# Kernel optimization log

Hardware: AMD Instinct MI355X
Metric: run time of the kernel (lower is better)

The kernel has to match this reference:

```python
import jax, jax.numpy as jnp
import numpy as np

BATCH, L = 2, 1024
D_MODEL, D_INNER, D_STATE, DT_RANK, K = 2048, 4096, 16, 128, 4


def setup_inputs() -> dict:
    key = jax.random.key(0)
    ks = jax.random.split(key, 9)
    g = lambda i, shape, s: jax.random.normal(ks[i], shape, jnp.float32) * s
    A_log = jnp.log(jnp.broadcast_to(jnp.arange(1, D_STATE + 1, dtype=jnp.float32),
                                     (D_INNER, D_STATE)))
    return {
        "hidden_states": g(0, (BATCH, L, D_MODEL), 1.0),
        "W_in": g(1, (2 * D_INNER, D_MODEL), 0.02),
        "conv_w": g(2, (D_INNER, K), 0.2),
        "conv_b": g(3, (D_INNER,), 0.02),
        "W_x": g(4, (DT_RANK + 2 * D_STATE, D_INNER), 0.02),
        "W_dt": g(5, (D_INNER, DT_RANK), 0.02),
        "b_dt": g(6, (D_INNER,), 0.02),
        "A_log": A_log,
        "D": jnp.ones((D_INNER,), jnp.float32),
        "W_out": g(7, (D_MODEL, D_INNER), 0.02),
        "b_out": g(8, (D_MODEL,), 0.02),
    }


def reference(hidden_states, W_in, conv_w, conv_b, W_x, W_dt, b_dt, A_log, D, W_out, b_out):
    b, l, _ = hidden_states.shape
    # in_proj -> (b, 2*d_inner, l), split into x and gate z
    xz = jnp.einsum('bld,ed->bel', hidden_states, W_in)
    x, z = jnp.split(xz, 2, axis=1)                      # each (b, d_inner, l)
    # conv_state = F.pad(x, (d_conv - l, 0)): keeps the last d_conv timesteps
    conv_state = x[:, :, -K:]
    # causal depthwise conv1d (left pad K-1) + SiLU
    xc = jax.lax.conv_general_dilated(
        x, conv_w[:, None, :], window_strides=(1,), padding=[(K - 1, 0)],
        feature_group_count=D_INNER, dimension_numbers=('NCH', 'OIH', 'NCH'))
    xc = jax.nn.silu(xc + conv_b[None, :, None])         # (b, d_inner, l)
    # x_proj -> dt / B / C
    x_dbl = jnp.einsum('bdl,ed->ble', xc, W_x)           # (b, l, dt_rank+2n)
    dt, Bm, Cm = jnp.split(x_dbl, [DT_RANK, DT_RANK + D_STATE], axis=-1)
    dt = jnp.einsum('blr,dr->bdl', dt, W_dt)             # (b, d_inner, l), no bias here
    delta = jax.nn.softplus(dt + b_dt[None, :, None])    # dt_proj bias folded into softplus
    A = -jnp.exp(A_log)                                  # (d_inner, d_state)

    def step(state, inp):                                # state: (b, d_inner, d_state)
        d_t, b_t, c_t, u_t = inp                         # (b,d), (b,n), (b,n), (b,d)
        dA = jnp.exp(d_t[..., None] * A)                 # (b, d, n)
        state = dA * state + (d_t * u_t)[..., None] * b_t[:, None, :]
        y_t = jnp.einsum('bdn,bn->bd', state, c_t)
        return state, y_t

    xs = (delta.transpose(2, 0, 1),                      # (l, b, d)
          Bm.transpose(1, 0, 2),                         # (l, b, n)
          Cm.transpose(1, 0, 2),
          xc.transpose(2, 0, 1))
    init = jnp.zeros((b, D_INNER, D_STATE), delta.dtype)
    last_state, ys = jax.lax.scan(step, init, xs)
    y = ys.transpose(1, 2, 0) + D[None, :, None] * xc    # (b, d_inner, l) skip term
    y = y * jax.nn.silu(z)                               # gating
    out = jnp.einsum('bdl,ed->ble', y, W_out) + b_out    # (b, l, d_model)
    return out, conv_state, last_state
```

## Files before the change

kernel.cpp:

```cpp
#include <hip/hip_runtime.h>
#include <stdint.h>
#include <stddef.h>

typedef __bf16 bf16;
typedef __attribute__((ext_vector_type(8))) __bf16 bf16x8;
typedef __attribute__((ext_vector_type(4))) float floatx4;

#define GAS __attribute__((address_space(1)))
#define LAS __attribute__((address_space(3)))

__device__ __forceinline__ void async16(const void* g, void* l) {
  __builtin_amdgcn_global_load_lds((const GAS void*)g, (LAS void*)l, 16, 0, 0);
}

__device__ __forceinline__ bf16x8 cvt8(const float* p) {
  floatx4 a = *(const floatx4*)p;
  floatx4 b = *(const floatx4*)(p + 4);
  bf16x8 r;
  r[0] = (bf16)a[0]; r[1] = (bf16)a[1]; r[2] = (bf16)a[2]; r[3] = (bf16)a[3];
  r[4] = (bf16)b[0]; r[5] = (bf16)b[1]; r[6] = (bf16)b[2]; r[7] = (bf16)b[3];
  return r;
}

__global__ __launch_bounds__(512, 2) void gemm256_8p(
    const bf16* __restrict__ A, const bf16* __restrict__ B,
    bf16* __restrict__ C, int M, int N, int K, int lda, int ldb) {
  __shared__ __attribute__((aligned(16))) bf16 SA[2][2][8192];
  __shared__ __attribute__((aligned(16))) bf16 SB[2][2][8192];

  const int tid = threadIdx.x;
  const int wave = tid >> 6;
  const int lane = tid & 63;
  const int lr = lane & 15;
  const int kg = lane >> 4;
  const int wm = (wave >> 2) * 128;
  const int wn = (wave & 3) * 64;

  const int tilesM = M >> 8;
  const int tm = blockIdx.x % tilesM;
  const int tn = blockIdx.x / tilesM;
  const int rowBase = tm * 256;
  const int colBase = tn * 256;

  const int srow = tid >> 2;
  const int ske = (tid & 3) << 3;
  const int skel = ske ^ (((srow >> 1) & 3) << 3);
  const size_t aRow0 = (size_t)(rowBase + srow) * lda;
  const size_t aRow1 = aRow0 + (size_t)128 * lda;
  const size_t bRow0 = (size_t)(colBase + srow) * ldb;
  const size_t bRow1 = bRow0 + (size_t)128 * ldb;

  const int NT = K >> 6;

  const int keSh = (kg << 3) ^ (((lr >> 1) & 3) << 3);

  floatx4 acc[8][4] = {};

  auto stA = [&](int buf, int kh, int kt) {
    const int gk = kt * 64 + kh * 32 + skel;
    bf16* d = &SA[buf][kh][0];
    async16(A + aRow0 + gk, d + tid * 8);
    async16(A + aRow1 + gk, d + 4096 + tid * 8);
  };
  auto stB = [&](int buf, int kh, int kt) {
    const int gk = kt * 64 + kh * 32 + skel;
    bf16* d = &SB[buf][kh][0];
    async16(B + bRow0 + gk, d + tid * 8);
    async16(B + bRow1 + gk, d + 4096 + tid * 8);
  };

  stB(0, 0, 0); stA(0, 0, 0); stB(0, 1, 0); stA(0, 1, 0);
  stB(1, 0, 1); stA(1, 0, 1); stB(1, 1, 1);
  asm volatile("s_waitcnt vmcnt(6)" ::: "memory");
  __builtin_amdgcn_s_barrier();

  bf16x8 bg[4], af[4];

#define PH(BUF, KH, MH, DOB, STG, VM)                                          \
  {                                                                            \
    const bf16* Ar_ = &SA[BUF][KH][0];                                         \
    if constexpr (DOB) {                                                       \
      const bf16* Br_ = &SB[BUF][KH][0];                                       \
      _Pragma("unroll") for (int n = 0; n < 4; ++n)                            \
          bg[n] = *(const bf16x8*)&Br_[(wn + n * 16 + lr) * 32 + keSh];        \
    }                                                                          \
    _Pragma("unroll") for (int m = 0; m < 4; ++m)                              \
        af[m] =                                                                \
            *(const bf16x8*)&Ar_[(wm + ((MH)*4 + m) * 16 + lr) * 32 + keSh];   \
    STG;                                                                       \
    __builtin_amdgcn_s_barrier();                                              \
    asm volatile("s_waitcnt lgkmcnt(0)" ::: "memory");                         \
    __builtin_amdgcn_sched_barrier(0);                                         \
    __builtin_amdgcn_s_setprio(1);                                             \
    _Pragma("unroll") for (int m = 0; m < 4; ++m)                              \
      _Pragma("unroll") for (int n = 0; n < 4; ++n)                            \
          acc[(MH)*4 + m][n] = __builtin_amdgcn_mfma_f32_16x16x32_bf16(        \
              af[m], bg[n], acc[(MH)*4 + m][n], 0, 0, 0);                      \
    __builtin_amdgcn_s_setprio(0);                                             \
    if constexpr (VM) asm volatile("s_waitcnt vmcnt(6)" ::: "memory");         \
    __builtin_amdgcn_s_barrier();                                              \
  }

  for (int it = 0; it < (NT >> 1); ++it) {
    const int T0 = it * 2;
    const int T1 = T0 + 1;
    const int s1 = (T0 + 2 < NT) ? T0 + 2 : NT - 1;
    const int s2 = (T1 + 2 < NT) ? T1 + 2 : NT - 1;

    PH(0, 0, 0, true,  stA(1, 1, T1), false)
    PH(0, 0, 1, false, stB(0, 0, s1), false)
    PH(0, 1, 0, true,  stA(0, 0, s1), false)
    PH(0, 1, 1, false, stB(0, 1, s1), true)
    PH(1, 0, 0, true,  stA(0, 1, s1), false)
    PH(1, 0, 1, false, stB(1, 0, s2), false)
    PH(1, 1, 0, true,  stA(1, 0, s2), false)
    PH(1, 1, 1, false, stB(1, 1, s2), true)
  }
#undef PH

  asm volatile("s_waitcnt vmcnt(0)" ::: "memory");

#pragma unroll
  for (int m = 0; m < 8; ++m) {
#pragma unroll
    for (int n = 0; n < 4; ++n) {
      const int col = colBase + wn + n * 16 + lr;
#pragma unroll
      for (int r = 0; r < 4; ++r) {
        const int row = rowBase + wm + m * 16 + kg * 4 + r;
        C[(size_t)row * N + col] = (bf16)acc[m][n][r];
      }
    }
  }
}

template <int EPI, int AF, int BF, int TM>
__global__ __launch_bounds__(256, 4) void gemm_bt(
    const void* __restrict__ Aptr, const void* __restrict__ Bptr,
    void* __restrict__ Cout, const float* __restrict__ bias,
    int M, int N, int K, int lda, int ldb) {
  __shared__ bf16 As[TM * 32];
  __shared__ bf16 Bs[128 * 32];
  const int tid = threadIdx.x;

  const int rowBase = blockIdx.x * TM;
  const int colBase = blockIdx.y * 128;
  const int kLen = K / gridDim.z;
  const int k0 = blockIdx.z * kLen;
  const int kIters = kLen / 32;

  const int sRow = tid >> 2;
  const int sCol = (tid & 3) << 3;
  const int wave = tid >> 6;
  const int lane = tid & 63;
  constexpr int MI = 4;
  constexpr int NJ = (TM == 128) ? 4 : 2;
  const int wm = (TM == 128) ? ((wave >> 1) << 6) : 0;
  const int wn = (TM == 128) ? ((wave & 1) << 6) : (wave << 5);
  const int lr = lane & 15;
  const int kg = lane >> 4;

  floatx4 acc[MI][NJ] = {};

  for (int kt = 0; kt < kIters; ++kt) {
    const int kk = k0 + kt * 32;
    __syncthreads();
    if constexpr (AF) {
      const float* pa =
          (const float*)Aptr + (size_t)(rowBase + sRow) * lda + kk + sCol;
      *(bf16x8*)&As[tid * 8] = cvt8(pa);
      if constexpr (TM == 128)
        *(bf16x8*)&As[2048 + tid * 8] = cvt8(pa + (size_t)64 * lda);
    } else {
      const bf16* pa =
          (const bf16*)Aptr + (size_t)(rowBase + sRow) * lda + kk + sCol;
      async16(pa, &As[tid * 8]);
      if constexpr (TM == 128)
        async16(pa + (size_t)64 * lda, &As[2048 + tid * 8]);
    }
    if constexpr (BF) {
      const float* pb =
          (const float*)Bptr + (size_t)(colBase + sRow) * ldb + kk + sCol;
      *(bf16x8*)&Bs[tid * 8] = cvt8(pb);
      *(bf16x8*)&Bs[2048 + tid * 8] = cvt8(pb + (size_t)64 * ldb);
    } else {
      const bf16* pb =
          (const bf16*)Bptr + (size_t)(colBase + sRow) * ldb + kk + sCol;
      async16(pb, &Bs[tid * 8]);
      async16(pb + (size_t)64 * ldb, &Bs[2048 + tid * 8]);
    }
    __syncthreads();

    bf16x8 af[MI], bg[NJ];
#pragma unroll
    for (int i = 0; i < MI; ++i)
      af[i] = *(const bf16x8*)&As[(wm + i * 16 + lr) * 32 + kg * 8];
#pragma unroll
    for (int j = 0; j < NJ; ++j)
      bg[j] = *(const bf16x8*)&Bs[(wn + j * 16 + lr) * 32 + kg * 8];
#pragma unroll
    for (int i = 0; i < MI; ++i)
#pragma unroll
      for (int j = 0; j < NJ; ++j)
        acc[i][j] = __builtin_amdgcn_mfma_f32_16x16x32_bf16(af[i], bg[j],
                                                            acc[i][j], 0, 0, 0);
  }

#pragma unroll
  for (int i = 0; i < MI; ++i) {
#pragma unroll
    for (int j = 0; j < NJ; ++j) {
      const int col = colBase + wn + j * 16 + lr;
      float bv = 0.f;
      if constexpr (EPI == 2 || EPI == 3) bv = bias[col];
#pragma unroll
      for (int r = 0; r < 4; ++r) {
        const int row = rowBase + wm + i * 16 + kg * 4 + r;
        const size_t idx = (size_t)row * N + col;
        float v = acc[i][j][r];
        if constexpr (EPI == 0) {
          ((bf16*)Cout)[idx] = (bf16)v;
        } else if constexpr (EPI == 1) {
          atomicAdd((float*)Cout + idx, v);
        } else if constexpr (EPI == 2) {
          v += bv;
          const float t = __expf(v);
          const float sp = (v > 20.f) ? v : __logf(1.f + t);
          ((bf16*)Cout)[idx] = (bf16)sp;
        } else if constexpr (EPI == 3) {
          ((float*)Cout)[idx] = v + bv;
        } else {
          ((float*)Cout)[(size_t)blockIdx.z * 524288 + idx] = v;
        }
      }
    }
  }
}

__global__ __launch_bounds__(256) void reduce_xdbl(
    const float* __restrict__ part, float* __restrict__ xdbl) {
  const size_t i4 = ((size_t)blockIdx.x * 256 + threadIdx.x) * 4;
  floatx4 s = {};
#pragma unroll
  for (int z = 0; z < 8; ++z) {
    const floatx4 v = *(const floatx4*)&part[(size_t)z * 524288 + i4];
    s[0] += v[0]; s[1] += v[1]; s[2] += v[2]; s[3] += v[3];
  }
  *(floatx4*)&xdbl[i4] = s;
}

#define PC0 524288UL
#define PC1 2621440UL
#define PC2 2686976UL
#define PC3 3735552UL
#define PC4 3866624UL
__global__ __launch_bounds__(256) void prep_all(
    const float* __restrict__ h, const float* __restrict__ wi,
    const float* __restrict__ wd, const float* __restrict__ wo,
    const float* __restrict__ wx, bf16* __restrict__ hb,
    bf16* __restrict__ wib, bf16* __restrict__ wdb, bf16* __restrict__ wob,
    bf16* __restrict__ wxp) {
  const size_t c = (size_t)blockIdx.x * 256 + threadIdx.x;
  if (c < PC0) {
    const size_t e = c * 8;
    *(bf16x8*)&hb[e] = cvt8(&h[e]);
  } else if (c < PC1) {
    const size_t e = (c - PC0) * 8;
    *(bf16x8*)&wib[e] = cvt8(&wi[e]);
  } else if (c < PC2) {
    const size_t e = (c - PC1) * 8;
    *(bf16x8*)&wdb[e] = cvt8(&wd[e]);
  } else if (c < PC3) {
    const size_t e = (c - PC2) * 8;
    *(bf16x8*)&wob[e] = cvt8(&wo[e]);
  } else if (c < PC4) {
    const size_t e = (c - PC3) * 8;
    if ((e >> 12) < 160) {
      *(bf16x8*)&wxp[e] = cvt8(&wx[e]);
    } else {
      bf16x8 z = {};
      *(bf16x8*)&wxp[e] = z;
    }
  }
}

__global__ void wxpad_prep(const float* __restrict__ Wx,
                           bf16* __restrict__ WXPAD) {
  const int idx = blockIdx.x * 256 + threadIdx.x;
  const int row = idx >> 12;
  WXPAD[idx] = (row < 160) ? (bf16)Wx[idx] : (bf16)0.f;
}

__global__ void conv_kernel(const bf16* __restrict__ XZ,
                            const float* __restrict__ conv_w,
                            const float* __restrict__ conv_b,
                            bf16* __restrict__ XC,
                            float* __restrict__ outConv) {
  const int idx = blockIdx.x * 256 + threadIdx.x;
  const int d = idx & 4095;
  const int row = idx >> 12;
  const int l = row & 1023;
  float acc = conv_b[d];
#pragma unroll
  for (int k = 0; k < 4; ++k) {
    if (l - 3 + k >= 0)
      acc += conv_w[d * 4 + k] * (float)XZ[(size_t)(row - 3 + k) * 8192 + d];
  }
  const float s = acc / (1.f + __expf(-acc));
  XC[(size_t)row * 4096 + d] = (bf16)s;
  if (idx < 32768) {
    const int k = idx & 3;
    const int dd = (idx >> 2) & 4095;
    const int b = idx >> 14;
    outConv[idx] = (float)XZ[(size_t)(b * 1024 + 1020 + k) * 8192 + dd];
  }
}

#define NCH 32
#define CLEN 32
#define LOG2E 1.44269504088896f

__global__ __launch_bounds__(256) void scan_phase1(
    const bf16* __restrict__ DELTA, const bf16* __restrict__ XC,
    const float* __restrict__ XDBL, const float* __restrict__ A_log,
    bf16* __restrict__ P, bf16* __restrict__ Lc) {
  const int bd = blockIdx.x * 256 + threadIdx.x;
  const int c = blockIdx.y;
  const int b = bd >> 12;
  const int d = bd & 4095;
  float A2[16], st[16], p[16];
#pragma unroll
  for (int n = 0; n < 16; ++n) {
    A2[n] = -__expf(A_log[d * 16 + n]) * LOG2E;
    st[n] = 0.f;
    p[n] = 1.f;
  }
  size_t row = (size_t)b * 1024 + (size_t)c * CLEN;
  for (int t = 0; t < CLEN; ++t, ++row) {
    const float dlt = (float)DELTA[row * 4096 + d];
    const float u = (float)XC[row * 4096 + d];
    const float* __restrict__ Bp = XDBL + row * 256 + 128;
    const float du = dlt * u;
#pragma unroll
    for (int n = 0; n < 16; ++n) {
      const float dA = exp2f(dlt * A2[n]);
      st[n] = dA * st[n] + du * Bp[n];
      p[n] *= dA;
    }
  }
  const size_t o = ((size_t)c * 8192 + bd) * 16;
  bf16x8 pk[2], lk[2];
#pragma unroll
  for (int n = 0; n < 16; ++n) {
    pk[n >> 3][n & 7] = (bf16)p[n];
    lk[n >> 3][n & 7] = (bf16)st[n];
  }
  *(bf16x8*)&P[o] = pk[0];
  *(bf16x8*)&P[o + 8] = pk[1];
  *(bf16x8*)&Lc[o] = lk[0];
  *(bf16x8*)&Lc[o + 8] = lk[1];
}

__global__ __launch_bounds__(256) void scan_phase2(
    const bf16* __restrict__ P, const bf16* __restrict__ Lc,
    float* __restrict__ In, float* __restrict__ lastOut) {
  const int bd = blockIdx.x * 256 + threadIdx.x;
  float st[16] = {};
  for (int c = 0; c < NCH; ++c) {
    const size_t o = ((size_t)c * 8192 + bd) * 16;
    const bf16x8 p0 = *(const bf16x8*)&P[o];
    const bf16x8 p1 = *(const bf16x8*)&P[o + 8];
    const bf16x8 l0 = *(const bf16x8*)&Lc[o];
    const bf16x8 l1 = *(const bf16x8*)&Lc[o + 8];
    floatx4 w[4];
#pragma unroll
    for (int n = 0; n < 16; ++n) w[n >> 2][n & 3] = st[n];
#pragma unroll
    for (int q = 0; q < 4; ++q) *(floatx4*)&In[o + q * 4] = w[q];
#pragma unroll
    for (int n = 0; n < 8; ++n) {
      st[n] = (float)p0[n] * st[n] + (float)l0[n];
      st[8 + n] = (float)p1[n] * st[8 + n] + (float)l1[n];
    }
  }
  const int b = bd >> 12;
  const int d = bd & 4095;
#pragma unroll
  for (int n = 0; n < 16; ++n)
    lastOut[(size_t)b * 65536 + d * 16 + n] = st[n];
}

__global__ __launch_bounds__(256) void scan_phase3(
    const bf16* __restrict__ DELTA, const bf16* __restrict__ XC,
    const bf16* __restrict__ XZ, const float* __restrict__ XDBL,
    const float* __restrict__ A_log, const float* __restrict__ Dp,
    const float* __restrict__ In, bf16* __restrict__ Y) {
  const int bd = blockIdx.x * 256 + threadIdx.x;
  const int c = blockIdx.y;
  const int b = bd >> 12;
  const int d = bd & 4095;
  float A2[16], st[16];
  const size_t o = ((size_t)c * 8192 + bd) * 16;
#pragma unroll
  for (int q = 0; q < 4; ++q) {
    const floatx4 v = *(const floatx4*)&In[o + q * 4];
#pragma unroll
    for (int j = 0; j < 4; ++j) st[q * 4 + j] = v[j];
  }
#pragma unroll
  for (int n = 0; n < 16; ++n)
    A2[n] = -__expf(A_log[d * 16 + n]) * LOG2E;
  const float Dd = Dp[d];
  size_t row = (size_t)b * 1024 + (size_t)c * CLEN;
  for (int t = 0; t < CLEN; ++t, ++row) {
    const float dlt = (float)DELTA[row * 4096 + d];
    const float u = (float)XC[row * 4096 + d];
    const float z = (float)XZ[row * 8192 + 4096 + d];
    const float* __restrict__ Bp = XDBL + row * 256 + 128;
    const float du = dlt * u;
    float y = 0.f;
#pragma unroll
    for (int n = 0; n < 16; ++n) {
      const float dA = exp2f(dlt * A2[n]);
      st[n] = dA * st[n] + du * Bp[n];
      y += st[n] * Bp[16 + n];
    }
    const float sig = 1.f / (1.f + __expf(-z));
    Y[row * 4096 + d] = (bf16)((y + Dd * u) * (z * sig));
  }
}

#define OFF_XZ 0UL
#define OFF_XC 33554432UL
#define OFF_DELTA 50331648UL
#define OFF_Y 83886080UL
#define OFF_XDBL 100663296UL
#define OFF_WXPAD 103284736UL
#define OFF_P 105381888UL
#define OFF_L 113770496UL
#define OFF_HBF 122159104UL
#define OFF_WINBF 130547712UL
#define OFF_WDTBF 164102144UL
#define OFF_WOUTBF 165150720UL
#define WS_NEED_CAST 181927936UL

extern "C" void kernel_launch(void* const* d_in, const int* in_sizes, int n_in,
                              void* d_out, int out_size, void* d_ws,
                              size_t ws_size, hipStream_t stream) {
  const float* hidden = (const float*)d_in[0];
  const float* W_in = (const float*)d_in[1];
  const float* conv_w = (const float*)d_in[2];
  const float* conv_b = (const float*)d_in[3];
  const float* W_x = (const float*)d_in[4];
  const float* W_dt = (const float*)d_in[5];
  const float* b_dt = (const float*)d_in[6];
  const float* A_log = (const float*)d_in[7];
  const float* Dvec = (const float*)d_in[8];
  const float* W_out = (const float*)d_in[9];
  const float* b_out = (const float*)d_in[10];

  char* ws = (char*)d_ws;
  bf16* XZ = (bf16*)(ws + OFF_XZ);
  bf16* XC = (bf16*)(ws + OFF_XC);
  bf16* DELTA = (bf16*)(ws + OFF_DELTA);
  float* PART = (float*)(ws + OFF_DELTA + 16777216UL);
  bf16* Y = (bf16*)(ws + OFF_Y);
  float* XDBL = (float*)(ws + OFF_XDBL);
  bf16* WXPAD = (bf16*)(ws + OFF_WXPAD);
  bf16* P = (bf16*)(ws + OFF_P);
  bf16* Lc = (bf16*)(ws + OFF_L);

  float* out = (float*)d_out;
  float* out_conv = out + 4194304;
  float* out_last = out + 4227072;
  float* In = out;

  const bool castOK = ws_size >= WS_NEED_CAST;
  if (castOK) {
    bf16* HBF = (bf16*)(ws + OFF_HBF);
    bf16* WINBF = (bf16*)(ws + OFF_WINBF);
    bf16* WDTBF = (bf16*)(ws + OFF_WDTBF);
    bf16* WOUTBF = (bf16*)(ws + OFF_WOUTBF);
    prep_all<<<15104, 256, 0, stream>>>(hidden, W_in, W_dt, W_out, W_x, HBF,
                                        WINBF, WDTBF, WOUTBF, WXPAD);
    gemm256_8p<<<dim3(256), 512, 0, stream>>>(HBF, WINBF, XZ, 2048, 8192,
                                              2048, 2048, 2048);
    conv_kernel<<<32768, 256, 0, stream>>>(XZ, conv_w, conv_b, XC, out_conv);
    gemm_bt<4, 0, 0, 64><<<dim3(32, 2, 8), 256, 0, stream>>>(
        XC, WXPAD, PART, nullptr, 2048, 256, 4096, 4096, 4096);
    reduce_xdbl<<<512, 256, 0, stream>>>(PART, XDBL);
    gemm_bt<2, 1, 0, 64><<<dim3(32, 32, 1), 256, 0, stream>>>(
        XDBL, WDTBF, DELTA, b_dt, 2048, 4096, 128, 256, 128);
    scan_phase1<<<dim3(32, NCH), 256, 0, stream>>>(DELTA, XC, XDBL, A_log, P,
                                                   Lc);
    scan_phase2<<<32, 256, 0, stream>>>(P, Lc, In, out_last);
    scan_phase3<<<dim3(32, NCH), 256, 0, stream>>>(DELTA, XC, XZ, XDBL, A_log,
                                                   Dvec, In, Y);
    gemm_bt<3, 0, 0, 64><<<dim3(32, 16, 1), 256, 0, stream>>>(
        Y, WOUTBF, out, b_out, 2048, 2048, 4096, 4096, 4096);
  } else {
    wxpad_prep<<<4096, 256, 0, stream>>>(W_x, WXPAD);
    gemm_bt<0, 1, 1, 128><<<dim3(16, 64, 1), 256, 0, stream>>>(
        hidden, W_in, XZ, nullptr, 2048, 8192, 2048, 2048, 2048);
    conv_kernel<<<32768, 256, 0, stream>>>(XZ, conv_w, conv_b, XC, out_conv);
    gemm_bt<4, 0, 0, 64><<<dim3(32, 2, 8), 256, 0, stream>>>(
        XC, WXPAD, PART, nullptr, 2048, 256, 4096, 4096, 4096);
    reduce_xdbl<<<512, 256, 0, stream>>>(PART, XDBL);
    gemm_bt<2, 1, 1, 64><<<dim3(32, 32, 1), 256, 0, stream>>>(
        XDBL, W_dt, DELTA, b_dt, 2048, 4096, 128, 256, 128);
    scan_phase1<<<dim3(32, NCH), 256, 0, stream>>>(DELTA, XC, XDBL, A_log, P,
                                                   Lc);
    scan_phase2<<<32, 256, 0, stream>>>(P, Lc, In, out_last);
    scan_phase3<<<dim3(32, NCH), 256, 0, stream>>>(DELTA, XC, XZ, XDBL, A_log,
                                                   Dvec, In, Y);
    gemm_bt<3, 0, 1, 64><<<dim3(32, 16, 1), 256, 0, stream>>>(
        Y, W_out, out, b_out, 2048, 2048, 4096, 4096, 4096);
  }
}
```

Baseline: 519.4 us.

## Double-buffer LDS fragment reads in in_proj GEMM and spread scan_phase2 across more blocks

The in_proj 256x256 GEMM now keeps two sets of A and B register fragments and issues the LDS reads for the next phase before waiting on the current one. It waits with partial lgkmcnt counts instead of draining to zero, so LDS read latency overlaps the MFMA work, and the vmcnt waits and prologue are adjusted to match. Separately, scan_phase2 goes from 32 blocks of 256 threads to 128 blocks of 64 threads so the sequential chunk combine spreads over more CUs. The cost is higher register pressure in the GEMM under its 512-thread, 2-block launch bounds, and the hand-tuned wait counts must stay correct or results break.

```diff
diff --git a/kernel.cpp b/kernel.cpp
--- a/kernel.cpp
+++ b/kernel.cpp
@@ -55,6 +55,7 @@
   const int keSh = (kg << 3) ^ (((lr >> 1) & 3) << 3);
 
   floatx4 acc[8][4] = {};
+  bf16x8 af0[4], af1[4], bgA[4], bgB[4];
 
   auto stA = [&](int buf, int kh, int kt) {
     const int gk = kt * 64 + kh * 32 + skel;
@@ -69,35 +70,37 @@
     async16(B + bRow1 + gk, d + 4096 + tid * 8);
   };
 
+#define RD_B(DST, BUF, KH)                                                     \
+  _Pragma("unroll") for (int n = 0; n < 4; ++n)                                \
+      DST[n] = *(const bf16x8*)&SB[BUF][KH][(wn + n * 16 + lr) * 32 + keSh];
+#define RD_A(DST, BUF, KH, MH)                                                 \
+  _Pragma("unroll") for (int m = 0; m < 4; ++m)                                \
+      DST[m] =                                                                 \
+          *(const bf16x8*)&SA[BUF][KH][(wm + ((MH)*4 + m) * 16 + lr) * 32 +    \
+                                       keSh];
+
   stB(0, 0, 0); stA(0, 0, 0); stB(0, 1, 0); stA(0, 1, 0);
+  asm volatile("s_waitcnt vmcnt(0)" ::: "memory");
+  __builtin_amdgcn_s_barrier();
   stB(1, 0, 1); stA(1, 0, 1); stB(1, 1, 1);
-  asm volatile("s_waitcnt vmcnt(6)" ::: "memory");
-  __builtin_amdgcn_s_barrier();
-
-  bf16x8 bg[4], af[4];
-
-#define PH(BUF, KH, MH, DOB, STG, VM)                                          \
+  RD_B(bgA, 0, 0);
+  RD_A(af0, 0, 0, 0);
+
+#define PH(RDS, CNT, STG, BGR, AFR, MH, VM)                                    \
   {                                                                            \
-    const bf16* Ar_ = &SA[BUF][KH][0];                                         \
-    if constexpr (DOB) {                                                       \
-      const bf16* Br_ = &SB[BUF][KH][0];                                       \
-      _Pragma("unroll") for (int n = 0; n < 4; ++n)                            \
-          bg[n] = *(const bf16x8*)&Br_[(wn + n * 16 + lr) * 32 + keSh];        \
-    }                                                                          \
-    _Pragma("unroll") for (int m = 0; m < 4; ++m)                              \
-        af[m] =                                                                \
-            *(const bf16x8*)&Ar_[(wm + ((MH)*4 + m) * 16 + lr) * 32 + keSh];   \
+    RDS;                                                                       \
     STG;                                                                       \
     __builtin_amdgcn_s_barrier();                                              \
-    asm volatile("s_waitcnt lgkmcnt(0)" ::: "memory");                         \
+    asm volatile("s_waitcnt lgkmcnt(" #CNT ")" ::: "memory");                  \
     __builtin_amdgcn_sched_barrier(0);                                         \
     __builtin_amdgcn_s_setprio(1);                                             \
     _Pragma("unroll") for (int m = 0; m < 4; ++m)                              \
       _Pragma("unroll") for (int n = 0; n < 4; ++n)                            \
           acc[(MH)*4 + m][n] = __builtin_amdgcn_mfma_f32_16x16x32_bf16(        \
-              af[m], bg[n], acc[(MH)*4 + m][n], 0, 0, 0);                      \
+              AFR[m], BGR[n], acc[(MH)*4 + m][n], 0, 0, 0);                    \
     __builtin_amdgcn_s_setprio(0);                                             \
-    if constexpr (VM) asm volatile("s_waitcnt vmcnt(6)" ::: "memory");         \
+    __builtin_amdgcn_sched_barrier(0);                                         \
+    if constexpr (VM) asm volatile("s_waitcnt vmcnt(8)" ::: "memory");         \
     __builtin_amdgcn_s_barrier();                                              \
   }
 
@@ -107,18 +110,24 @@
     const int s1 = (T0 + 2 < NT) ? T0 + 2 : NT - 1;
     const int s2 = (T1 + 2 < NT) ? T1 + 2 : NT - 1;
 
-    PH(0, 0, 0, true,  stA(1, 1, T1), false)
-    PH(0, 0, 1, false, stB(0, 0, s1), false)
-    PH(0, 1, 0, true,  stA(0, 0, s1), false)
-    PH(0, 1, 1, false, stB(0, 1, s1), true)
-    PH(1, 0, 0, true,  stA(0, 1, s1), false)
-    PH(1, 0, 1, false, stB(1, 0, s2), false)
-    PH(1, 1, 0, true,  stA(1, 0, s2), false)
-    PH(1, 1, 1, false, stB(1, 1, s2), true)
+    PH(RD_A(af1, 0, 0, 1), 4, stA(1, 1, T1), bgA, af0, 0, true)
+    PH(RD_B(bgB, 0, 1); RD_A(af0, 0, 1, 0), 8, stB(0, 0, s1), bgA, af1, 1,
+       false)
+    PH(RD_A(af1, 0, 1, 1), 4, stA(0, 0, s1), bgB, af0, 0, true)
+    PH(RD_B(bgA, 1, 0); RD_A(af0, 1, 0, 0), 8, stB(0, 1, s1), bgB, af1, 1,
+       false)
+    PH(RD_A(af1, 1, 0, 1), 4, stA(0, 1, s1), bgA, af0, 0, true)
+    PH(RD_B(bgB, 1, 1); RD_A(af0, 1, 1, 0), 8, stB(1, 0, s2), bgA, af1, 1,
+       false)
+    PH(RD_A(af1, 1, 1, 1), 4, stA(1, 0, s2), bgB, af0, 0, true)
+    PH(RD_B(bgA, 0, 0); RD_A(af0, 0, 0, 0), 8, stB(1, 1, s2), bgB, af1, 1,
+       false)
   }
 #undef PH
-
-  asm volatile("s_waitcnt vmcnt(0)" ::: "memory");
+#undef RD_A
+#undef RD_B
+
+  asm volatile("s_waitcnt vmcnt(0) lgkmcnt(0)" ::: "memory");
 
 #pragma unroll
   for (int m = 0; m < 8; ++m) {
@@ -361,10 +370,10 @@
   *(bf16x8*)&Lc[o + 8] = lk[1];
 }
 
-__global__ __launch_bounds__(256) void scan_phase2(
+__global__ __launch_bounds__(64) void scan_phase2(
     const bf16* __restrict__ P, const bf16* __restrict__ Lc,
     float* __restrict__ In, float* __restrict__ lastOut) {
-  const int bd = blockIdx.x * 256 + threadIdx.x;
+  const int bd = blockIdx.x * 64 + threadIdx.x;
   float st[16] = {};
   for (int c = 0; c < NCH; ++c) {
     const size_t o = ((size_t)c * 8192 + bd) * 16;
@@ -493,7 +502,7 @@
         XDBL, WDTBF, DELTA, b_dt, 2048, 4096, 128, 256, 128);
     scan_phase1<<<dim3(32, NCH), 256, 0, stream>>>(DELTA, XC, XDBL, A_log, P,
                                                    Lc);
-    scan_phase2<<<32, 256, 0, stream>>>(P, Lc, In, out_last);
+    scan_phase2<<<128, 64, 0, stream>>>(P, Lc, In, out_last);
     scan_phase3<<<dim3(32, NCH), 256, 0, stream>>>(DELTA, XC, XZ, XDBL, A_log,
                                                    Dvec, In, Y);
     gemm_bt<3, 0, 0, 64><<<dim3(32, 16, 1), 256, 0, stream>>>(
@@ -510,7 +519,7 @@
         XDBL, W_dt, DELTA, b_dt, 2048, 4096, 128, 256, 128);
     scan_phase1<<<dim3(32, NCH), 256, 0, stream>>>(DELTA, XC, XDBL, A_log, P,
                                                    Lc);
-    scan_phase2<<<32, 256, 0, stream>>>(P, Lc, In, out_last);
+    scan_phase2<<<128, 64, 0, stream>>>(P, Lc, In, out_last);
     scan_phase3<<<dim3(32, NCH), 256, 0, stream>>>(DELTA, XC, XZ, XDBL, A_log,
                                                    Dvec, In, Y);
     gemm_bt<3, 0, 1, 64><<<dim3(32, 16, 1), 256, 0, stream>>>(
```

After: 501.8 us. 3.4% less time.
